# Kernel optimization log

Measured on AMD Instinct MI355X. Metric: run time of the kernel, lower is better.

Reference implementation:

```python
import jax, jax.numpy as jnp
import numpy as np

NUM_HEADS = 16

def setup_inputs() -> dict:
    key = jax.random.key(0)
    k1, k2, k3 = jax.random.split(key, 3)
    B, N, D = 4, 2048, 1024
    init_attn_std = D ** (-0.5)
    x = jax.random.normal(k1, (B, N, D), dtype=jnp.float32)
    qkv_w = jax.random.normal(k2, (D, 3 * D), dtype=jnp.float32) * init_attn_std
    proj_w = jax.random.normal(k3, (D, D), dtype=jnp.float32) * init_attn_std
    proj_b = jnp.zeros((D,), dtype=jnp.float32)
    return {"x": x, "qkv_w": qkv_w, "proj_w": proj_w, "proj_b": proj_b}

def reference(x, qkv_w, proj_w, proj_b):
    B, N, D = x.shape
    H = NUM_HEADS
    hd = D // H
    scale = hd ** (-0.5)
    # QKV projection (no bias, qkv_bias=False)
    qkv = (x @ qkv_w).reshape(B, N, 3, H, hd)
    q, k, v = jnp.moveaxis(qkv, 2, 0)  # each [B, N, H, hd]
    # scaled dot-product attention with causal mask (matches flax nn.dot_product_attention)
    scores = jnp.einsum('bqhd,bkhd->bhqk', q * scale, k)  # [B, H, N, N]
    causal = jnp.tril(jnp.ones((N, N), dtype=bool))
    big_neg = jnp.finfo(scores.dtype).min
    scores = jnp.where(causal, scores, big_neg)
    attn = jax.nn.softmax(scores, axis=-1)
    out = jnp.einsum('bhqk,bkhd->bqhd', attn, v).reshape(B, N, D)
    # output projection (proj_bias=True)
    return out @ proj_w + proj_b
```

## Files before the change

### kernel.cpp

```cpp
#include <hip/hip_runtime.h>

typedef __attribute__((ext_vector_type(8))) short sh8;
typedef __attribute__((ext_vector_type(8))) __bf16 bf8v;
typedef __attribute__((ext_vector_type(4))) float f4v;
typedef __attribute__((ext_vector_type(16))) float f16v;
typedef __attribute__((ext_vector_type(4))) unsigned u4v;

__device__ __forceinline__ float fast_exp2(float x) { return __builtin_amdgcn_exp2f(x); }

__device__ __forceinline__ unsigned short f2bf(float f) {
  unsigned u = __builtin_bit_cast(unsigned, f);
  u += 0x7fffu + ((u >> 16) & 1u);
  return (unsigned short)(u >> 16);
}
__device__ __forceinline__ float bf2f(unsigned short h) {
  unsigned u = ((unsigned)h) << 16;
  return __builtin_bit_cast(float, u);
}

__device__ __forceinline__ void glds16(const unsigned short* g, unsigned short* l) {
  __builtin_amdgcn_global_load_lds((const __attribute__((address_space(1))) void*)g,
                                   (__attribute__((address_space(3))) void*)l, 16, 0, 0);
}

__global__ __launch_bounds__(256) void cast_kernel(const float* __restrict__ in,
                                                   unsigned short* __restrict__ out) {
  const int idx = (blockIdx.x * 256 + threadIdx.x) * 4;
  const float4 v = *(const float4*)(in + idx);
  ushort4 o;
  o.x = f2bf(v.x); o.y = f2bf(v.y); o.z = f2bf(v.z); o.w = f2bf(v.w);
  *(ushort4*)(out + idx) = o;
}

__global__ __launch_bounds__(256) void transpose_cast_kernel(const float* __restrict__ in,
                                                             unsigned short* __restrict__ out,
                                                             int R, int C) {
  __shared__ float tile[32][33];
  const int c0 = blockIdx.x * 32, r0 = blockIdx.y * 32;
  const int tx = threadIdx.x, ty = threadIdx.y;
#pragma unroll
  for (int i = 0; i < 4; ++i)
    tile[ty + 8 * i][tx] = in[(size_t)(r0 + ty + 8 * i) * C + c0 + tx];
  __syncthreads();
#pragma unroll
  for (int i = 0; i < 4; ++i)
    out[(size_t)(c0 + ty + 8 * i) * R + r0 + tx] = f2bf(tile[tx][ty + 8 * i]);
}

template <int MODE>
__global__ __launch_bounds__(256, MODE == 0 ? 4 : 2) void gemm_bf16_kernel(
    const unsigned short* __restrict__ A,
    const unsigned short* __restrict__ Bt,
    int M, int N, int K,
    unsigned short* __restrict__ q_out, unsigned short* __restrict__ k_out,
    unsigned short* __restrict__ v_out,
    const float* __restrict__ bias, float* __restrict__ c_out) {
  constexpr int SMEM_SH = (MODE == 0) ? (128 * 128) : (2 * 4 * 128 * 32);
  __shared__ alignas(16) unsigned short smem[SMEM_SH];
  const int tid = threadIdx.x;
  const int lane = tid & 63;
  const int wave = tid >> 6;
  const int wr = (wave >> 1) * 64;
  const int wc = (wave & 1) * 64;
  const int bm = blockIdx.x * 128;
  const int bn = blockIdx.y * 128;
  const int fr = lane & 15;
  const int kq = lane >> 4;

  f4v acc[4][4] = {};

  const int r16 = lane >> 2;
  const int srcsl = (lane & 3) ^ ((r16 >> 1) & 3);
  const int rb0 = wave * 32, rb1 = wave * 32 + 16;
  const int rsl = (kq ^ ((fr >> 1) & 3)) * 8;
  const int nT = K >> 5;

  if constexpr (MODE == 0) {
    unsigned short* As = smem;
    unsigned short* Bs = smem + 4096;
    for (int j = 0; j < nT; ++j) {
      const int k0 = j * 32;
      __syncthreads();
      glds16(&A[(size_t)(bm + rb0 + r16) * K + k0 + srcsl * 8], &As[rb0 * 32]);
      glds16(&A[(size_t)(bm + rb1 + r16) * K + k0 + srcsl * 8], &As[rb1 * 32]);
      glds16(&Bt[(size_t)(bn + rb0 + r16) * K + k0 + srcsl * 8], &Bs[rb0 * 32]);
      glds16(&Bt[(size_t)(bn + rb1 + r16) * K + k0 + srcsl * 8], &Bs[rb1 * 32]);
      __syncthreads();

      bf8v af[4], bfv[4];
#pragma unroll
      for (int m = 0; m < 4; ++m)
        af[m] = __builtin_bit_cast(bf8v, *(const sh8*)&As[(wr + m * 16 + fr) * 32 + rsl]);
#pragma unroll
      for (int n = 0; n < 4; ++n)
        bfv[n] = __builtin_bit_cast(bf8v, *(const sh8*)&Bs[(wc + n * 16 + fr) * 32 + rsl]);
      __builtin_amdgcn_s_setprio(1);
#pragma unroll
      for (int m = 0; m < 4; ++m)
#pragma unroll
        for (int n = 0; n < 4; ++n)
          acc[m][n] = __builtin_amdgcn_mfma_f32_16x16x32_bf16(af[m], bfv[n], acc[m][n], 0, 0, 0);
      __builtin_amdgcn_s_setprio(0);
    }

    if (blockIdx.y >= 16) {
      unsigned short* Vlds = smem;
      __syncthreads();
#pragma unroll
      for (int m = 0; m < 4; ++m)
#pragma unroll
        for (int n = 0; n < 4; ++n)
#pragma unroll
          for (int i = 0; i < 4; ++i) {
            const int rp = wr + m * 16 + kq * 4 + i;
            const int cp = wc + n * 16 + fr;
            Vlds[cp * 128 + (((rp >> 3) ^ (cp & 7)) << 3) + (rp & 7)] = f2bf(acc[m][n][i]);
          }
      __syncthreads();
      const int cp = tid >> 1, half = tid & 1;
      const int b = bm >> 11;
      const int h = ((bn - 2048) >> 6) + (cp >> 6);
      const int d = cp & 63;
      unsigned short* dst =
          v_out + ((size_t)((b * 16 + h) * 64 + d)) * 2048 + (bm & 2047) + half * 64;
#pragma unroll
      for (int s = 0; s < 8; ++s) {
        const int slot = (half * 8 + s) ^ (cp & 7);
        *(sh8*)(dst + s * 8) = *(const sh8*)&Vlds[cp * 128 + slot * 8];
      }
      return;
    }

#pragma unroll
    for (int m = 0; m < 4; ++m)
#pragma unroll
      for (int n = 0; n < 4; ++n)
#pragma unroll
        for (int i = 0; i < 4; ++i) {
          const int r = bm + wr + m * 16 + kq * 4 + i;
          const int c = bn + wc + n * 16 + fr;
          const float val = acc[m][n][i];
          const int b = r >> 11, nidx = r & 2047;
          const int rem = c & 1023;
          const int h = rem >> 6, d = rem & 63;
          const size_t off = ((size_t)((b * 16 + h) * 2048 + nidx)) * 64 + d;
          if (blockIdx.y < 8) q_out[off] = f2bf(val * 0.18033688f);
          else                k_out[off] = f2bf(val);
        }
  } else {
    unsigned short* As = smem;
    unsigned short* Bs = smem + 16384;
#define GSTAGE(g)                                                                            \
    {                                                                                        \
      const int _b = ((g) & 3) * 4096;                                                       \
      const int _k0 = (g) * 32;                                                              \
      glds16(&A[(size_t)(bm + rb0 + r16) * K + _k0 + srcsl * 8], &As[_b + rb0 * 32]);        \
      glds16(&A[(size_t)(bm + rb1 + r16) * K + _k0 + srcsl * 8], &As[_b + rb1 * 32]);        \
      glds16(&Bt[(size_t)(bn + rb0 + r16) * K + _k0 + srcsl * 8], &Bs[_b + rb0 * 32]);       \
      glds16(&Bt[(size_t)(bn + rb1 + r16) * K + _k0 + srcsl * 8], &Bs[_b + rb1 * 32]);       \
    }
    GSTAGE(0);
    GSTAGE(1);
    for (int j = 0; j < nT; ++j) {
      const int buf = (j & 3) * 4096;
      if (j + 2 < nT) {
        GSTAGE(j + 2);
        asm volatile("s_waitcnt vmcnt(8)" ::: "memory");
      } else if (j + 1 < nT) {
        asm volatile("s_waitcnt vmcnt(4)" ::: "memory");
      } else {
        asm volatile("s_waitcnt vmcnt(0)" ::: "memory");
      }
      __builtin_amdgcn_s_barrier();

      bf8v af[4], bfv[4];
#pragma unroll
      for (int m = 0; m < 4; ++m)
        af[m] = __builtin_bit_cast(bf8v, *(const sh8*)&As[buf + (wr + m * 16 + fr) * 32 + rsl]);
#pragma unroll
      for (int n = 0; n < 4; ++n)
        bfv[n] = __builtin_bit_cast(bf8v, *(const sh8*)&Bs[buf + (wc + n * 16 + fr) * 32 + rsl]);
      __builtin_amdgcn_s_setprio(1);
#pragma unroll
      for (int m = 0; m < 4; ++m)
#pragma unroll
        for (int n = 0; n < 4; ++n)
          acc[m][n] = __builtin_amdgcn_mfma_f32_16x16x32_bf16(af[m], bfv[n], acc[m][n], 0, 0, 0);
      __builtin_amdgcn_s_setprio(0);
    }
#undef GSTAGE

#pragma unroll
    for (int m = 0; m < 4; ++m)
#pragma unroll
      for (int n = 0; n < 4; ++n)
#pragma unroll
        for (int i = 0; i < 4; ++i) {
          const int r = bm + wr + m * 16 + kq * 4 + i;
          const int c = bn + wc + n * 16 + fr;
          c_out[(size_t)r * N + c] = acc[m][n][i] + bias[c];
        }
  }
}

__global__ __launch_bounds__(256, 2) void attn_kernel(
    const unsigned short* __restrict__ Q, const unsigned short* __restrict__ Kg,
    const unsigned short* __restrict__ Vtg, unsigned short* __restrict__ O) {
  __shared__ alignas(16) unsigned short Ks[4][64 * 64];
  __shared__ alignas(16) unsigned short Vts[4][64 * 64];
  const int tid = threadIdx.x;
  const int lane = tid & 63;
  const int w = tid >> 6;
  const int q31 = lane & 31, hi = lane >> 5;
  const int sw = (lane & 7) << 3;
  const int wg = (blockIdx.x & 7) * 64 + (blockIdx.x >> 3);
  const int bh = wg >> 3;
  const int pair = wg & 7;
  const int qtA = pair, qtB = 15 - pair;
  const unsigned short* Qb = Q + (size_t)bh * (2048 * 64);
  const unsigned short* Kb = Kg + (size_t)bh * (2048 * 64);
  const unsigned short* Vtb = Vtg + (size_t)bh * (64 * 2048);
  const int q0wA = qtA * 128 + w * 32;
  const int q0wB = qtB * 128 + w * 32;

  bf8v qfA[4], qfB[4];
#pragma unroll
  for (int dk = 0; dk < 4; ++dk) {
    qfA[dk] = __builtin_bit_cast(bf8v, *(const sh8*)&Qb[(size_t)(q0wA + q31) * 64 + 8 * hi + 16 * dk]);
    qfB[dk] = __builtin_bit_cast(bf8v, *(const sh8*)&Qb[(size_t)(q0wB + q31) * 64 + 8 * hi + 16 * dk]);
  }

  f16v oA0 = {}, oA1 = {}, oB0 = {}, oB1 = {};
  float mA = -1e30f, lA = 0.f, mB = -1e30f, lB = 0.f;

  const int r8 = lane >> 3;
  const int gslot = (lane & 7) ^ r8;
  const int rb0 = w * 16, rb1 = w * 16 + 8;

#define STAGE(g)                                                                              \
  {                                                                                           \
    const int _b = (g) & 3;                                                                   \
    glds16(&Kb[(size_t)((g) * 64 + rb0 + r8) * 64 + gslot * 8], &Ks[_b][rb0 * 64]);           \
    glds16(&Kb[(size_t)((g) * 64 + rb1 + r8) * 64 + gslot * 8], &Ks[_b][rb1 * 64]);           \
    glds16(&Vtb[(size_t)(rb0 + r8) * 2048 + (g) * 64 + gslot * 8], &Vts[_b][rb0 * 64]);       \
    glds16(&Vtb[(size_t)(rb1 + r8) * 2048 + (g) * 64 + gslot * 8], &Vts[_b][rb1 * 64]);       \
  }

  auto body = [&](int j, int buf, int q0w, bf8v (&qf)[4], f16v& o0, f16v& o1,
                  float& m_i, float& l_i) {
    f16v s0 = {}, s1 = {};
    __builtin_amdgcn_s_setprio(1);
#pragma unroll
    for (int dk = 0; dk < 4; ++dk) {
      const int col = (8 * hi + 16 * dk) ^ sw;
      const bf8v k0 = __builtin_bit_cast(bf8v, *(const sh8*)&Ks[buf][q31 * 64 + col]);
      const bf8v k1 = __builtin_bit_cast(bf8v, *(const sh8*)&Ks[buf][(32 + q31) * 64 + col]);
      s0 = __builtin_amdgcn_mfma_f32_32x32x16_bf16(k0, qf[dk], s0, 0, 0, 0);
      s1 = __builtin_amdgcn_mfma_f32_32x32x16_bf16(k1, qf[dk], s1, 0, 0, 0);
    }
    __builtin_amdgcn_s_setprio(0);

    const int qg = q0w + q31;
    if (j * 64 + 63 > q0w) {
#pragma unroll
      for (int r = 0; r < 16; ++r) {
        const int kl = j * 64 + (r & 3) + 8 * (r >> 2) + 4 * hi;
        if (kl > qg) s0[r] = -1e30f;
        if (kl + 32 > qg) s1[r] = -1e30f;
      }
    }

    float mx = -1e30f;
#pragma unroll
    for (int r = 0; r < 16; ++r) mx = fmaxf(mx, fmaxf(s0[r], s1[r]));
    mx = fmaxf(mx, __shfl_xor(mx, 32));

    if (!__all(mx - m_i <= 8.f)) {
      const float mn = fmaxf(m_i, mx);
      const float alpha = fast_exp2(m_i - mn);
      m_i = mn;
      l_i *= alpha;
#pragma unroll
      for (int r = 0; r < 16; ++r) {
        const float ar = __shfl(alpha, (r & 3) + 8 * (r >> 2) + 4 * hi);
        o0[r] *= ar;
        o1[r] *= ar;
      }
    }

    float ps = 0.f;
#pragma unroll
    for (int r = 0; r < 16; ++r) {
      s0[r] = fast_exp2(s0[r] - m_i);
      s1[r] = fast_exp2(s1[r] - m_i);
      ps += s0[r] + s1[r];
    }
    ps += __shfl_xor(ps, 32);
    l_i += ps;

    unsigned w0[8], w1[8];
#pragma unroll
    for (int jj = 0; jj < 8; ++jj) {
      asm("v_cvt_pk_bf16_f32 %0, %1, %2" : "=v"(w0[jj]) : "v"(s0[2 * jj]), "v"(s0[2 * jj + 1]));
      asm("v_cvt_pk_bf16_f32 %0, %1, %2" : "=v"(w1[jj]) : "v"(s1[2 * jj]), "v"(s1[2 * jj + 1]));
    }

#pragma unroll
    for (int ks = 0; ks < 4; ++ks) {
      const int j0 = 4 * (ks & 1);
      unsigned x0 = (ks < 2 ? w0[j0 + 0] : w1[j0 + 0]);
      unsigned y0 = (ks < 2 ? w0[j0 + 2] : w1[j0 + 2]);
      unsigned x1 = (ks < 2 ? w0[j0 + 1] : w1[j0 + 1]);
      unsigned y1 = (ks < 2 ? w0[j0 + 3] : w1[j0 + 3]);
      asm("v_permlane32_swap_b32 %0, %1" : "+v"(x0), "+v"(y0));
      asm("v_permlane32_swap_b32 %0, %1" : "+v"(x1), "+v"(y1));
      u4v pw;
      pw[0] = x0; pw[1] = x1; pw[2] = y0; pw[3] = y1;
      const bf8v pa = __builtin_bit_cast(bf8v, pw);

      const int colv = (8 * hi + 16 * ks) ^ sw;
      const bf8v vf0 = __builtin_bit_cast(bf8v, *(const sh8*)&Vts[buf][q31 * 64 + colv]);
      const bf8v vf1 = __builtin_bit_cast(bf8v, *(const sh8*)&Vts[buf][(32 + q31) * 64 + colv]);
      __builtin_amdgcn_s_setprio(1);
      o0 = __builtin_amdgcn_mfma_f32_32x32x16_bf16(pa, vf0, o0, 0, 0, 0);
      o1 = __builtin_amdgcn_mfma_f32_32x32x16_bf16(pa, vf1, o1, 0, 0, 0);
      __builtin_amdgcn_s_setprio(0);
    }
  };

  const int b = bh >> 4, h = bh & 15;
  auto epi = [&](int q0w, f16v& o0, f16v& o1, float l_i) {
    const float rl = 1.f / l_i;
#pragma unroll
    for (int r = 0; r < 16; ++r) {
      const int cr = (r & 3) + 8 * (r >> 2) + 4 * hi;
      const float lr = __shfl(rl, cr);
      const size_t base = ((size_t)(b * 2048 + q0w + cr)) * 1024 + h * 64 + q31;
      O[base] = f2bf(o0[r] * lr);
      O[base + 32] = f2bf(o1[r] * lr);
    }
  };

  const int nA = 2 * qtA + 2;
  const int nT = 2 * qtB + 2;

  STAGE(0);
  STAGE(1);

  for (int j = 0; j < nT; ++j) {
    const int buf = j & 3;
    if (j + 2 < nT) {
      STAGE(j + 2);
      asm volatile("s_waitcnt vmcnt(8)" ::: "memory");
    } else if (j + 1 < nT) {
      asm volatile("s_waitcnt vmcnt(4)" ::: "memory");
    } else {
      asm volatile("s_waitcnt vmcnt(0)" ::: "memory");
    }
    __builtin_amdgcn_s_barrier();

    if (j < nA) body(j, buf, q0wA, qfA, oA0, oA1, mA, lA);
    body(j, buf, q0wB, qfB, oB0, oB1, mB, lB);

    if (j == nA - 1) epi(q0wA, oA0, oA1, lA);
  }
#undef STAGE

  epi(q0wB, oB0, oB1, lB);
}

extern "C" void kernel_launch(void* const* d_in, const int* in_sizes, int n_in,
                              void* d_out, int out_size, void* d_ws, size_t ws_size,
                              hipStream_t stream) {
  const float* x      = (const float*)d_in[0];
  const float* qkv_w  = (const float*)d_in[1];
  const float* proj_w = (const float*)d_in[2];
  const float* proj_b = (const float*)d_in[3];
  float* out = (float*)d_out;

  unsigned short* ws = (unsigned short*)d_ws;
  const size_t NE = (size_t)8192 * 1024;
  unsigned short* xb     = ws;
  unsigned short* wqkvT  = xb + NE;
  unsigned short* wprojT = wqkvT + (size_t)3072 * 1024;
  unsigned short* qb     = wprojT + (size_t)1024 * 1024;
  unsigned short* kb     = qb + NE;
  unsigned short* vt     = kb + NE;
  unsigned short* ab     = xb;

  cast_kernel<<<8192, 256, 0, stream>>>(x, xb);
  transpose_cast_kernel<<<dim3(96, 32), dim3(32, 8), 0, stream>>>(qkv_w, wqkvT, 1024, 3072);
  transpose_cast_kernel<<<dim3(32, 32), dim3(32, 8), 0, stream>>>(proj_w, wprojT, 1024, 1024);

  gemm_bf16_kernel<0><<<dim3(64, 24), 256, 0, stream>>>(
      xb, wqkvT, 8192, 3072, 1024, qb, kb, vt, nullptr, nullptr);

  attn_kernel<<<512, 256, 0, stream>>>(qb, kb, vt, ab);

  gemm_bf16_kernel<1><<<dim3(64, 8), 256, 0, stream>>>(
      ab, wprojT, 8192, 1024, 1024, nullptr, nullptr, nullptr, proj_b, out);
}
```

Before: 172.0 us.

## Interleave two query tiles' attention stages and stage Q/K stores through LDS

The attention loop now runs the QK^T MFMAs for both query tiles (A and B) together, then both softmaxes, then the PV MFMAs. The K/V fragments loaded from LDS are shared between the two tiles. This is meant to give independent MFMA chains for latency hiding and to halve the LDS fragment reads. Separately, the QKV GEMM epilogue for Q and K now transposes through a swizzled LDS tile and writes 16-byte vectors, replacing scattered 2-byte global stores. The interleaving raises register pressure, since four score accumulators and four packed-P arrays are live at once, which risks spills or lower occupancy.

```diff
diff --git a/kernel.cpp b/kernel.cpp
--- a/kernel.cpp
+++ b/kernel.cpp
@@ -131,22 +131,34 @@
       return;
     }
 
-#pragma unroll
-    for (int m = 0; m < 4; ++m)
-#pragma unroll
-      for (int n = 0; n < 4; ++n)
-#pragma unroll
-        for (int i = 0; i < 4; ++i) {
-          const int r = bm + wr + m * 16 + kq * 4 + i;
-          const int c = bn + wc + n * 16 + fr;
-          const float val = acc[m][n][i];
-          const int b = r >> 11, nidx = r & 2047;
-          const int rem = c & 1023;
-          const int h = rem >> 6, d = rem & 63;
-          const size_t off = ((size_t)((b * 16 + h) * 2048 + nidx)) * 64 + d;
-          if (blockIdx.y < 8) q_out[off] = f2bf(val * 0.18033688f);
-          else                k_out[off] = f2bf(val);
-        }
+    {
+      unsigned short* T = smem;
+      __syncthreads();
+      const float qs = (blockIdx.y < 8) ? 0.18033688f : 1.f;
+      unsigned short* outp = (blockIdx.y < 8) ? q_out : k_out;
+#pragma unroll
+      for (int m = 0; m < 4; ++m)
+#pragma unroll
+        for (int n = 0; n < 4; ++n)
+#pragma unroll
+          for (int i = 0; i < 4; ++i) {
+            const int rp = wr + m * 16 + kq * 4 + i;
+            const int cp = wc + n * 16 + fr;
+            T[rp * 128 + ((((cp >> 3) ^ (rp & 7)) << 3) | (cp & 7))] =
+                f2bf(acc[m][n][i] * qs);
+          }
+      __syncthreads();
+      const int rp = tid >> 1, half = tid & 1;
+      const int r = bm + rp;
+      const int b = r >> 11, nidx = r & 2047;
+      const int h = ((bn & 1023) >> 6) + half;
+      unsigned short* dst = outp + ((size_t)((b * 16 + h) * 2048 + nidx)) * 64;
+#pragma unroll
+      for (int s = 0; s < 8; ++s) {
+        const int slot = (half * 8 + s) ^ (rp & 7);
+        *(sh8*)(dst + s * 8) = *(const sh8*)&T[rp * 128 + (slot << 3)];
+      }
+    }
   } else {
     unsigned short* As = smem;
     unsigned short* Bs = smem + 16384;
@@ -246,20 +258,8 @@
     glds16(&Vtb[(size_t)(rb1 + r8) * 2048 + (g) * 64 + gslot * 8], &Vts[_b][rb1 * 64]);       \
   }
 
-  auto body = [&](int j, int buf, int q0w, bf8v (&qf)[4], f16v& o0, f16v& o1,
-                  float& m_i, float& l_i) {
-    f16v s0 = {}, s1 = {};
-    __builtin_amdgcn_s_setprio(1);
-#pragma unroll
-    for (int dk = 0; dk < 4; ++dk) {
-      const int col = (8 * hi + 16 * dk) ^ sw;
-      const bf8v k0 = __builtin_bit_cast(bf8v, *(const sh8*)&Ks[buf][q31 * 64 + col]);
-      const bf8v k1 = __builtin_bit_cast(bf8v, *(const sh8*)&Ks[buf][(32 + q31) * 64 + col]);
-      s0 = __builtin_amdgcn_mfma_f32_32x32x16_bf16(k0, qf[dk], s0, 0, 0, 0);
-      s1 = __builtin_amdgcn_mfma_f32_32x32x16_bf16(k1, qf[dk], s1, 0, 0, 0);
-    }
-    __builtin_amdgcn_s_setprio(0);
-
+  auto softmax = [&](int j, int q0w, f16v& s0, f16v& s1, f16v& o0, f16v& o1,
+                     float& m_i, float& l_i, unsigned (&wo0)[8], unsigned (&wo1)[8]) {
     const int qg = q0w + q31;
     if (j * 64 + 63 > q0w) {
 #pragma unroll
@@ -269,12 +269,10 @@
         if (kl + 32 > qg) s1[r] = -1e30f;
       }
     }
-
     float mx = -1e30f;
 #pragma unroll
     for (int r = 0; r < 16; ++r) mx = fmaxf(mx, fmaxf(s0[r], s1[r]));
     mx = fmaxf(mx, __shfl_xor(mx, 32));
-
     if (!__all(mx - m_i <= 8.f)) {
       const float mn = fmaxf(m_i, mx);
       const float alpha = fast_exp2(m_i - mn);
@@ -287,7 +285,6 @@
         o1[r] *= ar;
       }
     }
-
     float ps = 0.f;
 #pragma unroll
     for (int r = 0; r < 16; ++r) {
@@ -297,35 +294,24 @@
     }
     ps += __shfl_xor(ps, 32);
     l_i += ps;
-
-    unsigned w0[8], w1[8];
 #pragma unroll
     for (int jj = 0; jj < 8; ++jj) {
-      asm("v_cvt_pk_bf16_f32 %0, %1, %2" : "=v"(w0[jj]) : "v"(s0[2 * jj]), "v"(s0[2 * jj + 1]));
-      asm("v_cvt_pk_bf16_f32 %0, %1, %2" : "=v"(w1[jj]) : "v"(s1[2 * jj]), "v"(s1[2 * jj + 1]));
-    }
-
-#pragma unroll
-    for (int ks = 0; ks < 4; ++ks) {
-      const int j0 = 4 * (ks & 1);
-      unsigned x0 = (ks < 2 ? w0[j0 + 0] : w1[j0 + 0]);
-      unsigned y0 = (ks < 2 ? w0[j0 + 2] : w1[j0 + 2]);
-      unsigned x1 = (ks < 2 ? w0[j0 + 1] : w1[j0 + 1]);
-      unsigned y1 = (ks < 2 ? w0[j0 + 3] : w1[j0 + 3]);
-      asm("v_permlane32_swap_b32 %0, %1" : "+v"(x0), "+v"(y0));
-      asm("v_permlane32_swap_b32 %0, %1" : "+v"(x1), "+v"(y1));
-      u4v pw;
-      pw[0] = x0; pw[1] = x1; pw[2] = y0; pw[3] = y1;
-      const bf8v pa = __builtin_bit_cast(bf8v, pw);
-
-      const int colv = (8 * hi + 16 * ks) ^ sw;
-      const bf8v vf0 = __builtin_bit_cast(bf8v, *(const sh8*)&Vts[buf][q31 * 64 + colv]);
-      const bf8v vf1 = __builtin_bit_cast(bf8v, *(const sh8*)&Vts[buf][(32 + q31) * 64 + colv]);
-      __builtin_amdgcn_s_setprio(1);
-      o0 = __builtin_amdgcn_mfma_f32_32x32x16_bf16(pa, vf0, o0, 0, 0, 0);
-      o1 = __builtin_amdgcn_mfma_f32_32x32x16_bf16(pa, vf1, o1, 0, 0, 0);
-      __builtin_amdgcn_s_setprio(0);
-    }
+      asm("v_cvt_pk_bf16_f32 %0, %1, %2" : "=v"(wo0[jj]) : "v"(s0[2 * jj]), "v"(s0[2 * jj + 1]));
+      asm("v_cvt_pk_bf16_f32 %0, %1, %2" : "=v"(wo1[jj]) : "v"(s1[2 * jj]), "v"(s1[2 * jj + 1]));
+    }
+  };
+
+  auto make_pa = [&](int ks, unsigned (&w0)[8], unsigned (&w1)[8]) -> bf8v {
+    const int j0 = 4 * (ks & 1);
+    unsigned x0 = (ks < 2 ? w0[j0 + 0] : w1[j0 + 0]);
+    unsigned y0 = (ks < 2 ? w0[j0 + 2] : w1[j0 + 2]);
+    unsigned x1 = (ks < 2 ? w0[j0 + 1] : w1[j0 + 1]);
+    unsigned y1 = (ks < 2 ? w0[j0 + 3] : w1[j0 + 3]);
+    asm("v_permlane32_swap_b32 %0, %1" : "+v"(x0), "+v"(y0));
+    asm("v_permlane32_swap_b32 %0, %1" : "+v"(x1), "+v"(y1));
+    u4v pw;
+    pw[0] = x0; pw[1] = x1; pw[2] = y0; pw[3] = y1;
+    return __builtin_bit_cast(bf8v, pw);
   };
 
   const int b = bh >> 4, h = bh & 15;
@@ -359,8 +345,49 @@
     }
     __builtin_amdgcn_s_barrier();
 
-    if (j < nA) body(j, buf, q0wA, qfA, oA0, oA1, mA, lA);
-    body(j, buf, q0wB, qfB, oB0, oB1, mB, lB);
+    const bool doA = (j < nA);
+
+    f16v sA0 = {}, sA1 = {}, sB0 = {}, sB1 = {};
+    __builtin_amdgcn_s_setprio(1);
+#pragma unroll
+    for (int dk = 0; dk < 4; ++dk) {
+      const int col = (8 * hi + 16 * dk) ^ sw;
+      const bf8v k0 = __builtin_bit_cast(bf8v, *(const sh8*)&Ks[buf][q31 * 64 + col]);
+      const bf8v k1 = __builtin_bit_cast(bf8v, *(const sh8*)&Ks[buf][(32 + q31) * 64 + col]);
+      if (doA) {
+        sA0 = __builtin_amdgcn_mfma_f32_32x32x16_bf16(k0, qfA[dk], sA0, 0, 0, 0);
+        sA1 = __builtin_amdgcn_mfma_f32_32x32x16_bf16(k1, qfA[dk], sA1, 0, 0, 0);
+      }
+      sB0 = __builtin_amdgcn_mfma_f32_32x32x16_bf16(k0, qfB[dk], sB0, 0, 0, 0);
+      sB1 = __builtin_amdgcn_mfma_f32_32x32x16_bf16(k1, qfB[dk], sB1, 0, 0, 0);
+    }
+    __builtin_amdgcn_s_setprio(0);
+
+    unsigned wA0[8], wA1[8], wB0[8], wB1[8];
+    if (doA) softmax(j, q0wA, sA0, sA1, oA0, oA1, mA, lA, wA0, wA1);
+    softmax(j, q0wB, sB0, sB1, oB0, oB1, mB, lB, wB0, wB1);
+
+#pragma unroll
+    for (int ks = 0; ks < 4; ++ks) {
+      const int colv = (8 * hi + 16 * ks) ^ sw;
+      const bf8v vf0 = __builtin_bit_cast(bf8v, *(const sh8*)&Vts[buf][q31 * 64 + colv]);
+      const bf8v vf1 = __builtin_bit_cast(bf8v, *(const sh8*)&Vts[buf][(32 + q31) * 64 + colv]);
+      const bf8v paB = make_pa(ks, wB0, wB1);
+      if (doA) {
+        const bf8v paA = make_pa(ks, wA0, wA1);
+        __builtin_amdgcn_s_setprio(1);
+        oA0 = __builtin_amdgcn_mfma_f32_32x32x16_bf16(paA, vf0, oA0, 0, 0, 0);
+        oA1 = __builtin_amdgcn_mfma_f32_32x32x16_bf16(paA, vf1, oA1, 0, 0, 0);
+        oB0 = __builtin_amdgcn_mfma_f32_32x32x16_bf16(paB, vf0, oB0, 0, 0, 0);
+        oB1 = __builtin_amdgcn_mfma_f32_32x32x16_bf16(paB, vf1, oB1, 0, 0, 0);
+        __builtin_amdgcn_s_setprio(0);
+      } else {
+        __builtin_amdgcn_s_setprio(1);
+        oB0 = __builtin_amdgcn_mfma_f32_32x32x16_bf16(paB, vf0, oB0, 0, 0, 0);
+        oB1 = __builtin_amdgcn_mfma_f32_32x32x16_bf16(paB, vf1, oB1, 0, 0, 0);
+        __builtin_amdgcn_s_setprio(0);
+      }
+    }
 
     if (j == nA - 1) epi(q0wA, oA0, oA1, lA);
   }
```

Measured after the change: 189.9 us. +10.4%, slower.
